# Performance work log

Hardware: AMD Instinct MI355X
Metric: run time of the kernel (lower is better)

## Reference

```python
import jax, jax.numpy as jnp
import numpy as np

N = 4096
IN_F = 512
OUT_F = 256
HEADS = 4
HEAD_DIM = OUT_F // HEADS


def setup_inputs() -> dict:
    key = jax.random.key(0)
    k_feat, k_adj, k_w, k_a = jax.random.split(key, 4)
    features = jax.random.normal(k_feat, (N, IN_F), dtype=jnp.float32)
    adj_matrix = jax.random.uniform(k_adj, (N, N), dtype=jnp.float32)
    # xavier-uniform-ish init scaled small
    W = jax.random.normal(k_w, (OUT_F, IN_F), dtype=jnp.float32) * (1.0 / np.sqrt(IN_F))
    a = jax.random.normal(k_a, (HEADS, 2 * HEAD_DIM), dtype=jnp.float32) * 0.1
    bias = jnp.zeros((OUT_F,), dtype=jnp.float32)
    return {"features": features, "adj_matrix": adj_matrix, "W": W, "a": a, "bias": bias}


def reference(features, adj_matrix, W, a, bias):
    n = features.shape[0]
    h = features @ W.T                      # [N, OUT_F]
    hh = h.reshape(n, HEADS, HEAD_DIM)      # [N, H, D]
    # e[i,j,h] = leaky_relu(<h_i, a[:, :D]> + <h_j, a[:, D:]>) -- additive decomposition
    e_src = jnp.einsum('nhd,hd->nh', hh, a[:, :HEAD_DIM])   # [N, H]
    e_dst = jnp.einsum('nhd,hd->nh', hh, a[:, HEAD_DIM:])   # [N, H]
    e = e_src[:, None, :] + e_dst[None, :, :]               # [N, N, H]
    e = jnp.where(e >= 0, e, 0.2 * e)                       # leaky_relu(0.2)
    mask = adj_matrix[:, :, None] > 0.1                     # [N, N, 1]
    e = jnp.where(mask, e, -jnp.inf)
    attention = jax.nn.softmax(e, axis=1)                   # softmax over j
    attention = jnp.nan_to_num(attention, nan=0.0)          # fully-masked rows -> 0
    attention_mean = attention.mean(axis=2)                 # [N, N]
    h_out = attention_mean @ h + bias                       # [N, OUT_F]
    return h_out
```

## Files before the change

### kernel.cpp

```cpp
#include <hip/hip_runtime.h>
#include <math.h>

#define NN      4096
#define INF_    512
#define OUTF    256
#define NHEAD   4
#define HDIM    64
#define KSPLIT  4

typedef __attribute__((ext_vector_type(8))) short  short8x;
typedef __attribute__((ext_vector_type(4))) float  float4x;
typedef __attribute__((ext_vector_type(2))) float  float2x;

__device__ __forceinline__ unsigned short f2bf(float x) {
    union { float f; unsigned int u; } c; c.f = x;
    unsigned int r = (c.u + 0x7FFFu + ((c.u >> 16) & 1u)) >> 16;
    return (unsigned short)r;
}
__device__ __forceinline__ unsigned int cvtpk_bf16(float lo, float hi) {
    unsigned int r;
    asm("v_cvt_pk_bf16_f32 %0, %1, %2" : "=v"(r) : "v"(lo), "v"(hi));
    return r;
}
__device__ __forceinline__ float2x bf2up(unsigned int u) {
    union { unsigned int x; float f; } lo, hi;
    lo.x = u << 16; hi.x = u & 0xFFFF0000u;
    float2x r; r[0] = lo.f; r[1] = hi.f; return r;
}
__device__ __forceinline__ float2x max2(float2x a, float2x b) {
    float2x r; r[0] = fmaxf(a[0], b[0]); r[1] = fmaxf(a[1], b[1]); return r;
}

__global__ __launch_bounds__(256) void k_cast(const float* __restrict__ feat,
                                              const float* __restrict__ W,
                                              const float* __restrict__ bias,
                                              unsigned short* __restrict__ featb,
                                              unsigned short* __restrict__ Wb,
                                              float* __restrict__ out) {
    const int b = blockIdx.x;
    const int tid = threadIdx.x;
    if (b >= 2176) {
        int idx = (b - 2176) * 1024 + tid * 4;
        float4x bv = *(const float4x*)(bias + ((tid * 4) & 255));
        *(float4x*)(out + idx) = bv;
        return;
    }
    const float* src;
    unsigned short* dst;
    int idx;
    if (b < 2048) { src = feat; dst = featb; idx = b * 1024 + tid * 4; }
    else          { src = W;    dst = Wb;    idx = (b - 2048) * 1024 + tid * 4; }
    float4x v = *(const float4x*)(src + idx);
    ushort4 u;
    u.x = f2bf(v[0]); u.y = f2bf(v[1]); u.z = f2bf(v[2]); u.w = f2bf(v[3]);
    *(ushort4*)(dst + idx) = u;
}

__global__ __launch_bounds__(256) void k_hedge(const unsigned short* __restrict__ featb,
                                               const unsigned short* __restrict__ Wb,
                                               const float* __restrict__ a,
                                               unsigned short* __restrict__ hT,
                                               float* __restrict__ es,
                                               unsigned short* __restrict__ Bt,
                                               unsigned short* __restrict__ Dt) {
    __shared__ __align__(16) unsigned short lds_f[32 * 40];
    __shared__ __align__(16) unsigned short lds_w[256 * 40];
    const int tid  = threadIdx.x;
    const int w    = tid >> 6;
    const int lane = tid & 63;
    const int lidx = lane & 15;
    const int quad = lane >> 4;
    const int i0   = blockIdx.x * 32;
    const int srf  = tid >> 3;
    const int skf  = (tid & 7) * 4;
    const int srw  = tid >> 2;
    const int skw  = (tid & 3) * 8;

    float4x acc[2][4];
    #pragma unroll
    for (int p = 0; p < 2; ++p)
        #pragma unroll
        for (int q = 0; q < 4; ++q)
            acc[p][q] = (float4x){0.f, 0.f, 0.f, 0.f};

    for (int kt = 0; kt < INF_; kt += 32) {
        __syncthreads();
        *(ushort4*)&lds_f[srf * 40 + skf] = *(const ushort4*)&featb[(size_t)(i0 + srf) * INF_ + kt + skf];
        #pragma unroll
        for (int itr = 0; itr < 4; ++itr) {
            int n = itr * 64 + srw;
            *(ushort4*)&lds_w[n * 40 + skw]     = *(const ushort4*)&Wb[(size_t)n * INF_ + kt + skw];
            *(ushort4*)&lds_w[n * 40 + skw + 4] = *(const ushort4*)&Wb[(size_t)n * INF_ + kt + skw + 4];
        }
        __syncthreads();
        short8x af[2], bw[4];
        #pragma unroll
        for (int t = 0; t < 2; ++t)
            af[t] = *(const short8x*)&lds_f[(t * 16 + lidx) * 40 + quad * 8];
        #pragma unroll
        for (int t = 0; t < 4; ++t)
            bw[t] = *(const short8x*)&lds_w[(w * 64 + t * 16 + lidx) * 40 + quad * 8];
        #pragma unroll
        for (int it = 0; it < 2; ++it)
            #pragma unroll
            for (int nt = 0; nt < 4; ++nt)
                acc[it][nt] = __builtin_amdgcn_mfma_f32_16x16x32_bf16(
                    af[it], bw[nt], acc[it][nt], 0, 0, 0);
    }
    #pragma unroll
    for (int it = 0; it < 2; ++it)
        #pragma unroll
        for (int nt = 0; nt < 4; ++nt) {
            int col = w * 64 + nt * 16 + lidx;
            int m0r = i0 + it * 16 + quad * 4;
            uint2 u;
            u.x = cvtpk_bf16(acc[it][nt][0], acc[it][nt][1]);
            u.y = cvtpk_bf16(acc[it][nt][2], acc[it][nt][3]);
            *(uint2*)&hT[(size_t)col * NN + m0r] = u;
        }
    float asrc[4], adst[4];
    #pragma unroll
    for (int nt = 0; nt < 4; ++nt) {
        asrc[nt] = a[w * 2 * HDIM + nt * 16 + lidx];
        adst[nt] = a[w * 2 * HDIM + HDIM + nt * 16 + lidx];
    }
    #pragma unroll
    for (int it = 0; it < 2; ++it)
        #pragma unroll
        for (int r = 0; r < 4; ++r) {
            float s = 0.f, d = 0.f;
            #pragma unroll
            for (int nt = 0; nt < 4; ++nt) {
                s += acc[it][nt][r] * asrc[nt];
                d += acc[it][nt][r] * adst[nt];
            }
            #pragma unroll
            for (int off = 1; off < 16; off <<= 1) {
                s += __shfl_xor(s, off);
                d += __shfl_xor(d, off);
            }
            if (lidx == 0) {
                int row = i0 + it * 16 + quad * 4 + r;
                es[row * NHEAD + w] = s;
                Bt[row * NHEAD + w] = f2bf(__expf(d));
                Dt[row * NHEAD + w] = f2bf(__expf(0.2f * d));
            }
        }
}

__global__ __launch_bounds__(256) void k_den(const float* __restrict__ adj,
                                             const float* __restrict__ es,
                                             const unsigned short* __restrict__ Bt,
                                             const unsigned short* __restrict__ Dt,
                                             float* __restrict__ cden) {
    __shared__ float red[4][4];
    __shared__ float cfs[4];
    const int tid = threadIdx.x;
    const int wv  = tid >> 6;
    const int lane = tid & 63;
    const int i = blockIdx.x;

    const float4x esv = ((const float4x*)es)[i];
    float2x A01, A23, C01, C23;
    A01[0] = __expf(esv[0]); A01[1] = __expf(esv[1]);
    A23[0] = __expf(esv[2]); A23[1] = __expf(esv[3]);
    C01[0] = __expf(0.2f * esv[0]); C01[1] = __expf(0.2f * esv[1]);
    C23[0] = __expf(0.2f * esv[2]); C23[1] = __expf(0.2f * esv[3]);

    const float4x* arow4 = (const float4x*)(adj + (size_t)i * NN);
    const uint4* B4 = (const uint4*)Bt;
    const uint4* D4 = (const uint4*)Dt;

    float2x den01 = (float2x){0.f, 0.f};
    float2x den23 = (float2x){0.f, 0.f};
    #pragma unroll
    for (int t = 0; t < 4; ++t) {
        int jv = t * 256 + tid;
        float4x av = arow4[jv];
        uint4 bu0 = B4[jv * 2], bu1 = B4[jv * 2 + 1];
        uint4 du0 = D4[jv * 2], du1 = D4[jv * 2 + 1];
        unsigned int bwv[8] = {bu0.x, bu0.y, bu0.z, bu0.w, bu1.x, bu1.y, bu1.z, bu1.w};
        unsigned int dwv[8] = {du0.x, du0.y, du0.z, du0.w, du1.x, du1.y, du1.z, du1.w};
        #pragma unroll
        for (int u = 0; u < 4; ++u) {
            float2x b01 = bf2up(bwv[u * 2]);
            float2x b23 = bf2up(bwv[u * 2 + 1]);
            float2x d01 = bf2up(dwv[u * 2]);
            float2x d23 = bf2up(dwv[u * 2 + 1]);
            float mf = (av[u] > 0.1f) ? 1.f : 0.f;
            float2x mf2; mf2[0] = mf; mf2[1] = mf;
            den01 += mf2 * max2(A01 * b01, C01 * d01);
            den23 += mf2 * max2(A23 * b23, C23 * d23);
        }
    }
    float dh[4] = {den01[0], den01[1], den23[0], den23[1]};
    #pragma unroll
    for (int off = 1; off < 64; off <<= 1) {
        #pragma unroll
        for (int h = 0; h < 4; ++h)
            dh[h] += __shfl_xor(dh[h], off);
    }
    if (lane == 0) {
        #pragma unroll
        for (int h = 0; h < 4; ++h) red[wv][h] = dh[h];
    }
    __syncthreads();
    if (tid < 4)
        cfs[tid] = red[0][tid] + red[1][tid] + red[2][tid] + red[3][tid];
    __syncthreads();
    if (tid == 0) {
        float A[4] = {A01[0], A01[1], A23[0], A23[1]};
        float C[4] = {C01[0], C01[1], C23[0], C23[1]};
        float4x cA, cC;
        #pragma unroll
        for (int h = 0; h < 4; ++h) {
            float den = cfs[h];
            float sc = den > 0.f ? 0.25f / den : 0.f;
            cA[h] = A[h] * sc;
            cC[h] = C[h] * sc;
        }
        ((float4x*)cden)[i * 2]     = cA;
        ((float4x*)cden)[i * 2 + 1] = cC;
    }
}

__global__ __launch_bounds__(256) void k_fused(const float* __restrict__ adj,
                                               const float* __restrict__ cden,
                                               const unsigned short* __restrict__ Bt,
                                               const unsigned short* __restrict__ Dt,
                                               const unsigned short* __restrict__ hT,
                                               float* __restrict__ out) {
    __shared__ __align__(16) unsigned short lds_p[32 * 72];
    __shared__ __align__(16) unsigned short lds_h[256 * 72];
    const int tid  = threadIdx.x;
    const int w    = tid >> 6;
    const int lane = tid & 63;
    const int lidx = lane & 15;
    const int quad = lane >> 4;
    const int i0    = blockIdx.x * 32;
    const int kbase = blockIdx.y * (NN / KSPLIT);
    const int sr   = tid >> 3;
    const int sc8  = (tid & 7) * 8;

    const float4x cAv = ((const float4x*)cden)[(i0 + sr) * 2];
    const float4x cCv = ((const float4x*)cden)[(i0 + sr) * 2 + 1];
    float2x cA01, cA23, cC01, cC23;
    cA01[0] = cAv[0]; cA01[1] = cAv[1]; cA23[0] = cAv[2]; cA23[1] = cAv[3];
    cC01[0] = cCv[0]; cC01[1] = cCv[1]; cC23[0] = cCv[2]; cC23[1] = cCv[3];

    const uint4* B4 = (const uint4*)Bt;
    const uint4* D4 = (const uint4*)Dt;

    float4x acc[2][4];
    #pragma unroll
    for (int p = 0; p < 2; ++p)
        #pragma unroll
        for (int q = 0; q < 4; ++q)
            acc[p][q] = (float4x){0.f, 0.f, 0.f, 0.f};

    short8x pb[8];
    short8x pp;

    auto COMPP = [&](int ks) {
        const int jb = kbase + ks * 64 + sc8;
        float4x a0 = *(const float4x*)&adj[(size_t)(i0 + sr) * NN + jb];
        float4x a1 = *(const float4x*)&adj[(size_t)(i0 + sr) * NN + jb + 4];
        uint4 bu0 = B4[jb >> 1], bu1 = B4[(jb >> 1) + 1];
        uint4 bu2 = B4[(jb >> 1) + 2], bu3 = B4[(jb >> 1) + 3];
        uint4 du0 = D4[jb >> 1], du1 = D4[(jb >> 1) + 1];
        uint4 du2 = D4[(jb >> 1) + 2], du3 = D4[(jb >> 1) + 3];
        unsigned int bw[16] = {bu0.x, bu0.y, bu0.z, bu0.w, bu1.x, bu1.y, bu1.z, bu1.w,
                               bu2.x, bu2.y, bu2.z, bu2.w, bu3.x, bu3.y, bu3.z, bu3.w};
        unsigned int dw[16] = {du0.x, du0.y, du0.z, du0.w, du1.x, du1.y, du1.z, du1.w,
                               du2.x, du2.y, du2.z, du2.w, du3.x, du3.y, du3.z, du3.w};
        float pv[8];
        #pragma unroll
        for (int jj = 0; jj < 8; ++jj) {
            float2x b01 = bf2up(bw[jj * 2]);
            float2x b23 = bf2up(bw[jj * 2 + 1]);
            float2x d01 = bf2up(dw[jj * 2]);
            float2x d23 = bf2up(dw[jj * 2 + 1]);
            float2x t01 = max2(cA01 * b01, cC01 * d01);
            float2x t23 = max2(cA23 * b23, cC23 * d23);
            float av = (jj < 4) ? a0[jj] : a1[jj - 4];
            float s = (t01[0] + t01[1]) + (t23[0] + t23[1]);
            pv[jj] = (av > 0.1f) ? s : 0.f;
        }
        union { short8x s; unsigned int u[4]; } pk;
        pk.u[0] = cvtpk_bf16(pv[0], pv[1]);
        pk.u[1] = cvtpk_bf16(pv[2], pv[3]);
        pk.u[2] = cvtpk_bf16(pv[4], pv[5]);
        pk.u[3] = cvtpk_bf16(pv[6], pv[7]);
        pp = pk.s;
    };
    auto LOADB = [&](int ks) {
        const int ko = kbase + ks * 64;
        #pragma unroll
        for (int p = 0; p < 8; ++p)
            pb[p] = *(const short8x*)&hT[(size_t)(p * 32 + sr) * NN + ko + sc8];
    };

    LOADB(0);
    COMPP(0);

    const int KSTEPS = (NN / KSPLIT) / 64;
    for (int ks = 0; ks < KSTEPS; ++ks) {
        __syncthreads();
        *(short8x*)&lds_p[sr * 72 + sc8] = pp;
        #pragma unroll
        for (int p = 0; p < 8; ++p)
            *(short8x*)&lds_h[(p * 32 + sr) * 72 + sc8] = pb[p];
        __syncthreads();
        if (ks + 1 < KSTEPS) {
            LOADB(ks + 1);
            COMPP(ks + 1);
        }
        #pragma unroll
        for (int kk = 0; kk < 2; ++kk) {
            short8x af[2], bfr[4];
            #pragma unroll
            for (int it = 0; it < 2; ++it)
                af[it]  = *(const short8x*)&lds_p[(it * 16 + lidx) * 72 + kk * 32 + quad * 8];
            #pragma unroll
            for (int nt = 0; nt < 4; ++nt)
                bfr[nt] = *(const short8x*)&lds_h[(w * 64 + nt * 16 + lidx) * 72 + kk * 32 + quad * 8];
            #pragma unroll
            for (int it = 0; it < 2; ++it)
                #pragma unroll
                for (int nt = 0; nt < 4; ++nt)
                    acc[it][nt] = __builtin_amdgcn_mfma_f32_16x16x32_bf16(
                        af[it], bfr[nt], acc[it][nt], 0, 0, 0);
        }
    }
    #pragma unroll
    for (int it = 0; it < 2; ++it)
        #pragma unroll
        for (int nt = 0; nt < 4; ++nt)
            #pragma unroll
            for (int rr = 0; rr < 4; ++rr) {
                int row = i0 + it * 16 + quad * 4 + rr;
                int col = w * 64 + nt * 16 + lidx;
                unsafeAtomicAdd(&out[(size_t)row * OUTF + col], acc[it][nt][rr]);
            }
}

extern "C" void kernel_launch(void* const* d_in, const int* in_sizes, int n_in,
                              void* d_out, int out_size, void* d_ws, size_t ws_size,
                              hipStream_t stream) {
    const float* feat = (const float*)d_in[0];
    const float* adj  = (const float*)d_in[1];
    const float* W    = (const float*)d_in[2];
    const float* a    = (const float*)d_in[3];
    const float* bias = (const float*)d_in[4];
    float* out = (float*)d_out;

    char* ws = (char*)d_ws;
    float*          es    = (float*)(ws + 0);
    unsigned short* Btb   = (unsigned short*)(ws + (64u << 10));
    unsigned short* Dtb   = (unsigned short*)(ws + (96u << 10));
    float*          cden  = (float*)(ws + (128u << 10));
    unsigned short* hT    = (unsigned short*)(ws + (256u << 10));
    unsigned short* featb = (unsigned short*)(ws + (2560u << 10));
    unsigned short* Wb    = (unsigned short*)(ws + (6656u << 10));

    k_cast <<<3200,              256, 0, stream>>>(feat, W, bias, featb, Wb, out);
    k_hedge<<<128,               256, 0, stream>>>(featb, Wb, a, hT, es, Btb, Dtb);
    k_den  <<<NN,                256, 0, stream>>>(adj, es, Btb, Dtb, cden);
    k_fused<<<dim3(128, KSPLIT), 256, 0, stream>>>(adj, cden, Btb, Dtb, hT, out);
}
```

Measured before the change: 177.2 us.

## Fuse bf16 cast into projection GEMM, double k-split, defer P computation after MFMA

Removes the separate cast kernel. The projection kernel now reads fp32 features and W directly, converts them to bf16 while staging into LDS, and initializes the output with bias. The projection tile shrinks to 16 rows with a 64-wide k-step, which gives 256 blocks. The fused attention kernel doubles KSPLIT to 8 for more parallelism, and splits P computation into an early load and a math step run after the MFMAs so loads overlap compute. The cost is redundant fp32 W reads and conversion in every block, plus more atomic adds on the output.

```diff
diff --git a/kernel.cpp b/kernel.cpp
--- a/kernel.cpp
+++ b/kernel.cpp
@@ -6,7 +6,7 @@
 #define OUTF    256
 #define NHEAD   4
 #define HDIM    64
-#define KSPLIT  4
+#define KSPLIT  8
 
 typedef __attribute__((ext_vector_type(8))) short  short8x;
 typedef __attribute__((ext_vector_type(4))) float  float4x;
@@ -31,93 +31,88 @@
     float2x r; r[0] = fmaxf(a[0], b[0]); r[1] = fmaxf(a[1], b[1]); return r;
 }
 
-__global__ __launch_bounds__(256) void k_cast(const float* __restrict__ feat,
-                                              const float* __restrict__ W,
-                                              const float* __restrict__ bias,
-                                              unsigned short* __restrict__ featb,
-                                              unsigned short* __restrict__ Wb,
-                                              float* __restrict__ out) {
-    const int b = blockIdx.x;
-    const int tid = threadIdx.x;
-    if (b >= 2176) {
-        int idx = (b - 2176) * 1024 + tid * 4;
-        float4x bv = *(const float4x*)(bias + ((tid * 4) & 255));
-        *(float4x*)(out + idx) = bv;
-        return;
-    }
-    const float* src;
-    unsigned short* dst;
-    int idx;
-    if (b < 2048) { src = feat; dst = featb; idx = b * 1024 + tid * 4; }
-    else          { src = W;    dst = Wb;    idx = (b - 2048) * 1024 + tid * 4; }
-    float4x v = *(const float4x*)(src + idx);
-    ushort4 u;
-    u.x = f2bf(v[0]); u.y = f2bf(v[1]); u.z = f2bf(v[2]); u.w = f2bf(v[3]);
-    *(ushort4*)(dst + idx) = u;
-}
-
-__global__ __launch_bounds__(256) void k_hedge(const unsigned short* __restrict__ featb,
-                                               const unsigned short* __restrict__ Wb,
+__global__ __launch_bounds__(256) void k_hedge(const float* __restrict__ feat,
+                                               const float* __restrict__ W,
                                                const float* __restrict__ a,
+                                               const float* __restrict__ bias,
                                                unsigned short* __restrict__ hT,
                                                float* __restrict__ es,
                                                unsigned short* __restrict__ Bt,
-                                               unsigned short* __restrict__ Dt) {
-    __shared__ __align__(16) unsigned short lds_f[32 * 40];
-    __shared__ __align__(16) unsigned short lds_w[256 * 40];
+                                               unsigned short* __restrict__ Dt,
+                                               float* __restrict__ out) {
+    __shared__ __align__(16) unsigned short lds_f[16 * 72];
+    __shared__ __align__(16) unsigned short lds_w[256 * 72];
     const int tid  = threadIdx.x;
     const int w    = tid >> 6;
     const int lane = tid & 63;
     const int lidx = lane & 15;
     const int quad = lane >> 4;
-    const int i0   = blockIdx.x * 32;
-    const int srf  = tid >> 3;
-    const int skf  = (tid & 7) * 4;
-    const int srw  = tid >> 2;
-    const int skw  = (tid & 3) * 8;
-
-    float4x acc[2][4];
-    #pragma unroll
-    for (int p = 0; p < 2; ++p)
-        #pragma unroll
-        for (int q = 0; q < 4; ++q)
-            acc[p][q] = (float4x){0.f, 0.f, 0.f, 0.f};
-
-    for (int kt = 0; kt < INF_; kt += 32) {
+    const int i0   = blockIdx.x * 16;
+
+    {
+        float4x bv = *(const float4x*)(bias + ((tid * 4) & 255));
+        float* ob = out + (size_t)i0 * OUTF;
+        #pragma unroll
+        for (int itr = 0; itr < 4; ++itr)
+            *(float4x*)(ob + itr * 1024 + tid * 4) = bv;
+    }
+
+    const int fr = tid >> 4;
+    const int fc = (tid & 15) * 4;
+    const int wr = tid >> 2;
+    const int wc = (tid & 3) * 16;
+
+    float4x acc[4];
+    #pragma unroll
+    for (int q = 0; q < 4; ++q)
+        acc[q] = (float4x){0.f, 0.f, 0.f, 0.f};
+
+    for (int kt = 0; kt < INF_; kt += 64) {
         __syncthreads();
-        *(ushort4*)&lds_f[srf * 40 + skf] = *(const ushort4*)&featb[(size_t)(i0 + srf) * INF_ + kt + skf];
-        #pragma unroll
-        for (int itr = 0; itr < 4; ++itr) {
-            int n = itr * 64 + srw;
-            *(ushort4*)&lds_w[n * 40 + skw]     = *(const ushort4*)&Wb[(size_t)n * INF_ + kt + skw];
-            *(ushort4*)&lds_w[n * 40 + skw + 4] = *(const ushort4*)&Wb[(size_t)n * INF_ + kt + skw + 4];
+        {
+            float4x v = *(const float4x*)&feat[(size_t)(i0 + fr) * INF_ + kt + fc];
+            uint2 u;
+            u.x = cvtpk_bf16(v[0], v[1]);
+            u.y = cvtpk_bf16(v[2], v[3]);
+            *(uint2*)&lds_f[fr * 72 + fc] = u;
+        }
+        #pragma unroll
+        for (int p = 0; p < 4; ++p) {
+            int row = p * 64 + wr;
+            const float* src = &W[(size_t)row * INF_ + kt + wc];
+            float4x v0 = *(const float4x*)(src);
+            float4x v1 = *(const float4x*)(src + 4);
+            float4x v2 = *(const float4x*)(src + 8);
+            float4x v3 = *(const float4x*)(src + 12);
+            union { short8x s; unsigned int u[4]; } p0, p1;
+            p0.u[0] = cvtpk_bf16(v0[0], v0[1]); p0.u[1] = cvtpk_bf16(v0[2], v0[3]);
+            p0.u[2] = cvtpk_bf16(v1[0], v1[1]); p0.u[3] = cvtpk_bf16(v1[2], v1[3]);
+            p1.u[0] = cvtpk_bf16(v2[0], v2[1]); p1.u[1] = cvtpk_bf16(v2[2], v2[3]);
+            p1.u[2] = cvtpk_bf16(v3[0], v3[1]); p1.u[3] = cvtpk_bf16(v3[2], v3[3]);
+            *(short8x*)&lds_w[row * 72 + wc]     = p0.s;
+            *(short8x*)&lds_w[row * 72 + wc + 8] = p1.s;
         }
         __syncthreads();
-        short8x af[2], bw[4];
-        #pragma unroll
-        for (int t = 0; t < 2; ++t)
-            af[t] = *(const short8x*)&lds_f[(t * 16 + lidx) * 40 + quad * 8];
-        #pragma unroll
-        for (int t = 0; t < 4; ++t)
-            bw[t] = *(const short8x*)&lds_w[(w * 64 + t * 16 + lidx) * 40 + quad * 8];
-        #pragma unroll
-        for (int it = 0; it < 2; ++it)
+        #pragma unroll
+        for (int kk = 0; kk < 2; ++kk) {
+            short8x af = *(const short8x*)&lds_f[lidx * 72 + kk * 32 + quad * 8];
+            short8x bw[4];
             #pragma unroll
             for (int nt = 0; nt < 4; ++nt)
-                acc[it][nt] = __builtin_amdgcn_mfma_f32_16x16x32_bf16(
-                    af[it], bw[nt], acc[it][nt], 0, 0, 0);
-    }
-    #pragma unroll
-    for (int it = 0; it < 2; ++it)
-        #pragma unroll
-        for (int nt = 0; nt < 4; ++nt) {
-            int col = w * 64 + nt * 16 + lidx;
-            int m0r = i0 + it * 16 + quad * 4;
-            uint2 u;
-            u.x = cvtpk_bf16(acc[it][nt][0], acc[it][nt][1]);
-            u.y = cvtpk_bf16(acc[it][nt][2], acc[it][nt][3]);
-            *(uint2*)&hT[(size_t)col * NN + m0r] = u;
-        }
+                bw[nt] = *(const short8x*)&lds_w[(w * 64 + nt * 16 + lidx) * 72 + kk * 32 + quad * 8];
+            #pragma unroll
+            for (int nt = 0; nt < 4; ++nt)
+                acc[nt] = __builtin_amdgcn_mfma_f32_16x16x32_bf16(af, bw[nt], acc[nt], 0, 0, 0);
+        }
+    }
+    #pragma unroll
+    for (int nt = 0; nt < 4; ++nt) {
+        int col = w * 64 + nt * 16 + lidx;
+        uint2 u;
+        u.x = cvtpk_bf16(acc[nt][0], acc[nt][1]);
+        u.y = cvtpk_bf16(acc[nt][2], acc[nt][3]);
+        *(uint2*)&hT[(size_t)col * NN + i0 + quad * 4] = u;
+    }
     float asrc[4], adst[4];
     #pragma unroll
     for (int nt = 0; nt < 4; ++nt) {
@@ -125,27 +120,25 @@
         adst[nt] = a[w * 2 * HDIM + HDIM + nt * 16 + lidx];
     }
     #pragma unroll
-    for (int it = 0; it < 2; ++it)
-        #pragma unroll
-        for (int r = 0; r < 4; ++r) {
-            float s = 0.f, d = 0.f;
-            #pragma unroll
-            for (int nt = 0; nt < 4; ++nt) {
-                s += acc[it][nt][r] * asrc[nt];
-                d += acc[it][nt][r] * adst[nt];
-            }
-            #pragma unroll
-            for (int off = 1; off < 16; off <<= 1) {
-                s += __shfl_xor(s, off);
-                d += __shfl_xor(d, off);
-            }
-            if (lidx == 0) {
-                int row = i0 + it * 16 + quad * 4 + r;
-                es[row * NHEAD + w] = s;
-                Bt[row * NHEAD + w] = f2bf(__expf(d));
-                Dt[row * NHEAD + w] = f2bf(__expf(0.2f * d));
-            }
-        }
+    for (int r = 0; r < 4; ++r) {
+        float s = 0.f, d = 0.f;
+        #pragma unroll
+        for (int nt = 0; nt < 4; ++nt) {
+            s += acc[nt][r] * asrc[nt];
+            d += acc[nt][r] * adst[nt];
+        }
+        #pragma unroll
+        for (int off = 1; off < 16; off <<= 1) {
+            s += __shfl_xor(s, off);
+            d += __shfl_xor(d, off);
+        }
+        if (lidx == 0) {
+            int row = i0 + quad * 4 + r;
+            es[row * NHEAD + w] = s;
+            Bt[row * NHEAD + w] = f2bf(__expf(d));
+            Dt[row * NHEAD + w] = f2bf(__expf(0.2f * d));
+        }
+    }
 }
 
 __global__ __launch_bounds__(256) void k_den(const float* __restrict__ adj,
@@ -260,15 +253,25 @@
 
     short8x pb[8];
     short8x pp;
-
-    auto COMPP = [&](int ks) {
+    float4x a0, a1;
+    uint4 bu0, bu1, bu2, bu3, du0, du1, du2, du3;
+
+    auto LOADB = [&](int ks) {
+        const int ko = kbase + ks * 64;
+        #pragma unroll
+        for (int p = 0; p < 8; ++p)
+            pb[p] = *(const short8x*)&hT[(size_t)(p * 32 + sr) * NN + ko + sc8];
+    };
+    auto ALOAD = [&](int ks) {
         const int jb = kbase + ks * 64 + sc8;
-        float4x a0 = *(const float4x*)&adj[(size_t)(i0 + sr) * NN + jb];
-        float4x a1 = *(const float4x*)&adj[(size_t)(i0 + sr) * NN + jb + 4];
-        uint4 bu0 = B4[jb >> 1], bu1 = B4[(jb >> 1) + 1];
-        uint4 bu2 = B4[(jb >> 1) + 2], bu3 = B4[(jb >> 1) + 3];
-        uint4 du0 = D4[jb >> 1], du1 = D4[(jb >> 1) + 1];
-        uint4 du2 = D4[(jb >> 1) + 2], du3 = D4[(jb >> 1) + 3];
+        a0 = *(const float4x*)&adj[(size_t)(i0 + sr) * NN + jb];
+        a1 = *(const float4x*)&adj[(size_t)(i0 + sr) * NN + jb + 4];
+        bu0 = B4[jb >> 1]; bu1 = B4[(jb >> 1) + 1];
+        bu2 = B4[(jb >> 1) + 2]; bu3 = B4[(jb >> 1) + 3];
+        du0 = D4[jb >> 1]; du1 = D4[(jb >> 1) + 1];
+        du2 = D4[(jb >> 1) + 2]; du3 = D4[(jb >> 1) + 3];
+    };
+    auto PMATH = [&]() {
         unsigned int bw[16] = {bu0.x, bu0.y, bu0.z, bu0.w, bu1.x, bu1.y, bu1.z, bu1.w,
                                bu2.x, bu2.y, bu2.z, bu2.w, bu3.x, bu3.y, bu3.z, bu3.w};
         unsigned int dw[16] = {du0.x, du0.y, du0.z, du0.w, du1.x, du1.y, du1.z, du1.w,
@@ -293,15 +296,8 @@
         pk.u[3] = cvtpk_bf16(pv[6], pv[7]);
         pp = pk.s;
     };
-    auto LOADB = [&](int ks) {
-        const int ko = kbase + ks * 64;
-        #pragma unroll
-        for (int p = 0; p < 8; ++p)
-            pb[p] = *(const short8x*)&hT[(size_t)(p * 32 + sr) * NN + ko + sc8];
-    };
-
-    LOADB(0);
-    COMPP(0);
+
+    LOADB(0); ALOAD(0); PMATH();
 
     const int KSTEPS = (NN / KSPLIT) / 64;
     for (int ks = 0; ks < KSTEPS; ++ks) {
@@ -313,7 +309,7 @@
         __syncthreads();
         if (ks + 1 < KSTEPS) {
             LOADB(ks + 1);
-            COMPP(ks + 1);
+            ALOAD(ks + 1);
         }
         #pragma unroll
         for (int kk = 0; kk < 2; ++kk) {
@@ -331,6 +327,8 @@
                     acc[it][nt] = __builtin_amdgcn_mfma_f32_16x16x32_bf16(
                         af[it], bfr[nt], acc[it][nt], 0, 0, 0);
         }
+        if (ks + 1 < KSTEPS)
+            PMATH();
     }
     #pragma unroll
     for (int it = 0; it < 2; ++it)
@@ -360,11 +358,8 @@
     unsigned short* Dtb   = (unsigned short*)(ws + (96u << 10));
     float*          cden  = (float*)(ws + (128u << 10));
     unsigned short* hT    = (unsigned short*)(ws + (256u << 10));
-    unsigned short* featb = (unsigned short*)(ws + (2560u << 10));
-    unsigned short* Wb    = (unsigned short*)(ws + (6656u << 10));
-
-    k_cast <<<3200,              256, 0, stream>>>(feat, W, bias, featb, Wb, out);
-    k_hedge<<<128,               256, 0, stream>>>(featb, Wb, a, hT, es, Btb, Dtb);
+
+    k_hedge<<<256,               256, 0, stream>>>(feat, W, a, bias, hT, es, Btb, Dtb, out);
     k_den  <<<NN,                256, 0, stream>>>(adj, es, Btb, Dtb, cden);
     k_fused<<<dim3(128, KSPLIT), 256, 0, stream>>>(adj, cden, Btb, Dtb, hT, out);
 }
```

Measured after the change: 190.2 us. 7.3% more time.
